# Performance work log

Hardware: AMD Instinct MI355X
Metric: run time of the kernel (lower is better)

Reference implementation:

```python
import jax, jax.numpy as jnp
import numpy as np

N_NODES = 50000
N_EDGES = 800000
IN_FEATS = 128
HEADS = 8
OUT_FEATS = 32
NEG_SLOPE = 0.2


def setup_inputs() -> dict:
    key = jax.random.key(0)
    k_feat, k_w, k_al, k_ar, k_src, k_dst = jax.random.split(key, 6)
    feat = jax.random.normal(k_feat, (N_NODES, IN_FEATS), dtype=jnp.float32)
    W_fc = jax.random.normal(k_w, (HEADS * OUT_FEATS, IN_FEATS), dtype=jnp.float32) * 0.1
    attn_l = jax.random.normal(k_al, (1, HEADS, OUT_FEATS), dtype=jnp.float32) * 0.1
    attn_r = jax.random.normal(k_ar, (1, HEADS, OUT_FEATS), dtype=jnp.float32) * 0.1
    src = jax.random.randint(k_src, (N_EDGES,), 0, N_NODES, dtype=jnp.int32)
    dst = jax.random.randint(k_dst, (N_EDGES,), 0, N_NODES, dtype=jnp.int32)
    return {"feat": feat, "W_fc": W_fc, "attn_l": attn_l, "attn_r": attn_r,
            "src": src, "dst": dst}


def reference(feat, W_fc, attn_l, attn_r, src, dst):
    N = feat.shape[0]
    H, D = attn_l.shape[1], attn_l.shape[2]
    # fc projection: [N, H, D]
    feat_hd = (feat @ W_fc.T).reshape(N, H, D)
    # per-node left/right attention logits: [N, H]
    el = (feat_hd * attn_l).sum(-1)
    er = (feat_hd * attn_r).sum(-1)
    # u_add_v gather -> per-edge score [E, H], then leaky relu
    e = el[src] + er[dst]
    e = jnp.where(e > 0, e, NEG_SLOPE * e)
    # edge softmax: segment softmax over edges grouped by dst node
    m = jax.ops.segment_max(e, dst, num_segments=N)        # [N, H]
    a = jnp.exp(e - m[dst])                                # [E, H]
    z = jax.ops.segment_sum(a, dst, num_segments=N)        # [N, H]
    a = a / z[dst]
    # u_mul_e + sum: weighted scatter-aggregation -> [N, H, D]
    msg = feat_hd[src] * a[:, :, None]                     # [E, H, D]
    out = jax.ops.segment_sum(msg, dst, num_segments=N)
    return out
```

## Files before the change

### kernel.cpp

```cpp
#include <hip/hip_runtime.h>

#define N_NODES_C 50000
#define N_EDGES_C 800000
#define IN_FEATS_C 128
#define HEADS_C 8
#define HD_C 256
#define NEG_SLOPE_C 0.2f
#define SCAN_NBLK 49
#define LDT 136

#define GEMM_BLOCKS 782
#define DEG_BLOCKS 242
#define K1_GRID (GEMM_BLOCKS + DEG_BLOCKS)

typedef __attribute__((ext_vector_type(8))) short bf16x8;
typedef __attribute__((ext_vector_type(4))) float floatx4;

__device__ inline unsigned short f2bf(float f) {
  unsigned int u = __float_as_uint(f);
  unsigned int r = (u + 0x7FFFu + ((u >> 16) & 1u)) >> 16;
  return (unsigned short)r;
}
__device__ inline float bf2f(unsigned short s) {
  unsigned int u = ((unsigned int)s) << 16;
  return __uint_as_float(u);
}

__device__ inline void boff_scan(const int* __restrict__ bsum, int* sboff) {
  int t = threadIdx.x;
  if (t < 64) {
    int own = (t < SCAN_NBLK) ? bsum[t] : 0;
    int v = own;
#pragma unroll
    for (int off = 1; off < 64; off <<= 1) {
      int u = __shfl_up(v, off);
      if (t >= off) v += u;
    }
    sboff[t] = v - own;
  }
  __syncthreads();
}

__global__ __launch_bounds__(256) void prep_kernel(
    const float* __restrict__ W, unsigned short* __restrict__ Wbf,
    int* __restrict__ deg) {
  int b = blockIdx.x, t = threadIdx.x;
  if (b < 32) {
    int i = (b * 256 + t) * 4;
    float4 v = *(const float4*)&W[i];
    ushort4 o;
    o.x = f2bf(v.x); o.y = f2bf(v.y); o.z = f2bf(v.z); o.w = f2bf(v.w);
    *(ushort4*)&Wbf[i] = o;
  } else {
    int i = ((b - 32) * 256 + t) * 4;
    if (i < N_NODES_C) {
      if (i + 4 <= N_NODES_C)
        *(int4*)&deg[i] = make_int4(0, 0, 0, 0);
      else
        for (int k = i; k < N_NODES_C; ++k) deg[k] = 0;
    }
  }
}

__global__ __launch_bounds__(256) void front_kernel(
    const float* __restrict__ feat, const unsigned short* __restrict__ Wbf,
    const float* __restrict__ attn_l, const float* __restrict__ attn_r,
    const int* __restrict__ dst,
    unsigned short* __restrict__ feat_hd_bf,
    float* __restrict__ el, float* __restrict__ er,
    int* __restrict__ deg, int* __restrict__ rank) {
  __shared__ __align__(16) unsigned short sA[128 * LDT];
  __shared__ float sAttnL[128];
  __shared__ float sAttnR[128];
  const int bid = blockIdx.x;
  const int t = threadIdx.x;

  if (bid < DEG_BLOCKS) {
    for (int e0 = (bid * 256 + t) * 8; e0 < N_EDGES_C; e0 += DEG_BLOCKS * 2048) {
      int4 da = *(const int4*)&dst[e0];
      int4 db = *(const int4*)&dst[e0 + 4];
      int r0 = atomicAdd(&deg[da.x], 1);
      int r1 = atomicAdd(&deg[da.y], 1);
      int r2 = atomicAdd(&deg[da.z], 1);
      int r3 = atomicAdd(&deg[da.w], 1);
      int r4 = atomicAdd(&deg[db.x], 1);
      int r5 = atomicAdd(&deg[db.y], 1);
      int r6 = atomicAdd(&deg[db.z], 1);
      int r7 = atomicAdd(&deg[db.w], 1);
      *(int4*)&rank[e0]     = make_int4(r0, r1, r2, r3);
      *(int4*)&rank[e0 + 4] = make_int4(r4, r5, r6, r7);
    }
    return;
  }

  const int gb = bid - DEG_BLOCKS;
  int mt, nt;
  if (gb < 768) {
    mt = ((gb >> 4) << 3) + (gb & 7);
    nt = (gb >> 3) & 1;
  } else {
    int l = gb - 768;
    nt = (l >= 7) ? 1 : 0;
    mt = 384 + (nt ? l - 7 : l);
  }
  const int m0 = mt * 128;
  const int n0 = nt * 128;

  if (t < 128) {
    sAttnL[t] = attn_l[n0 + t];
    sAttnR[t] = attn_r[n0 + t];
  }
#pragma unroll
  for (int i = 0; i < 16; ++i) {
    int idx = t + i * 256;
    int row = idx >> 5;
    int c4 = idx & 31;
    int gn = m0 + row;
    float4 v = (gn < N_NODES_C)
                   ? *(const float4*)&feat[(size_t)gn * IN_FEATS_C + c4 * 4]
                   : make_float4(0.f, 0.f, 0.f, 0.f);
    ushort4 b;
    b.x = f2bf(v.x); b.y = f2bf(v.y); b.z = f2bf(v.z); b.w = f2bf(v.w);
    *(ushort4*)&sA[row * LDT + c4 * 4] = b;
  }
  __syncthreads();

  const int wid = t >> 6;
  const int lane = t & 63;
  const int quad = lane >> 4;
  const int l16 = lane & 15;
  const int wm = (wid & 1) * 64;
  const int wn = (wid >> 1) * 64;

  floatx4 acc[4][4];
#pragma unroll
  for (int i = 0; i < 4; ++i)
#pragma unroll
    for (int j = 0; j < 4; ++j) acc[i][j] = (floatx4){0.f, 0.f, 0.f, 0.f};

#pragma unroll
  for (int ks = 0; ks < 4; ++ks) {
    int k0 = ks * 32 + quad * 8;
    bf16x8 bfv[4];
#pragma unroll
    for (int n2 = 0; n2 < 4; ++n2)
      bfv[n2] = *(const bf16x8*)&Wbf[(size_t)(n0 + wn + n2 * 16 + l16) *
                                         IN_FEATS_C + k0];
    bf16x8 af[4];
#pragma unroll
    for (int m2 = 0; m2 < 4; ++m2)
      af[m2] = *(const bf16x8*)&sA[(wm + m2 * 16 + l16) * LDT + k0];
#pragma unroll
    for (int m2 = 0; m2 < 4; ++m2)
#pragma unroll
      for (int n2 = 0; n2 < 4; ++n2)
        acc[m2][n2] = __builtin_amdgcn_mfma_f32_16x16x32_bf16(
            af[m2], bfv[n2], acc[m2][n2], 0, 0, 0);
  }
  __syncthreads();

#pragma unroll
  for (int m2 = 0; m2 < 4; ++m2)
#pragma unroll
    for (int n2 = 0; n2 < 4; ++n2)
#pragma unroll
      for (int r = 0; r < 4; ++r) {
        int row = wm + m2 * 16 + quad * 4 + r;
        int col = wn + n2 * 16 + l16;
        sA[row * LDT + col] = f2bf(acc[m2][n2][r]);
      }
  __syncthreads();

#pragma unroll
  for (int i = 0; i < 8; ++i) {
    int idx = t + i * 256;
    int row = idx >> 4;
    int ch = idx & 15;
    int gn = m0 + row;
    if (gn < N_NODES_C) {
      *(uint4*)&feat_hd_bf[(size_t)gn * HD_C + n0 + ch * 8] =
          *(const uint4*)&sA[row * LDT + ch * 8];
    }
  }

  {
    int row = t >> 1;
    int hh = t & 1;
    int gn = m0 + row;
    if (gn < N_NODES_C) {
      const unsigned short* pr = &sA[row * LDT + hh * 64];
      const float* al = &sAttnL[hh * 64];
      const float* ar = &sAttnR[hh * 64];
      float el0 = 0.f, el1 = 0.f, er0 = 0.f, er1 = 0.f;
#pragma unroll
      for (int d8 = 0; d8 < 4; ++d8) {
        bf16x8 v0 = *(const bf16x8*)&pr[d8 * 8];
        bf16x8 v1 = *(const bf16x8*)&pr[32 + d8 * 8];
#pragma unroll
        for (int j = 0; j < 8; ++j) {
          float f0 = bf2f((unsigned short)v0[j]);
          float f1 = bf2f((unsigned short)v1[j]);
          el0 = fmaf(f0, al[d8 * 8 + j], el0);
          er0 = fmaf(f0, ar[d8 * 8 + j], er0);
          el1 = fmaf(f1, al[32 + d8 * 8 + j], el1);
          er1 = fmaf(f1, ar[32 + d8 * 8 + j], er1);
        }
      }
      int gh = nt * 4 + hh * 2;
      el[gn * HEADS_C + gh + 0] = el0;
      el[gn * HEADS_C + gh + 1] = el1;
      er[gn * HEADS_C + gh + 0] = er0;
      er[gn * HEADS_C + gh + 1] = er1;
    }
  }
}

__global__ __launch_bounds__(256) void scan1_kernel(
    const int* __restrict__ deg, int2* __restrict__ rsd,
    int* __restrict__ bsum) {
  __shared__ int s[256];
  int b = blockIdx.x, t = threadIdx.x;
  int i0 = b * 1024 + t * 4;
  int d0 = 0, d1 = 0, d2 = 0, d3 = 0;
  if (i0 + 4 <= N_NODES_C) {
    int4 d = *(const int4*)&deg[i0];
    d0 = d.x; d1 = d.y; d2 = d.z; d3 = d.w;
  } else {
    if (i0 + 0 < N_NODES_C) d0 = deg[i0 + 0];
    if (i0 + 1 < N_NODES_C) d1 = deg[i0 + 1];
    if (i0 + 2 < N_NODES_C) d2 = deg[i0 + 2];
    if (i0 + 3 < N_NODES_C) d3 = deg[i0 + 3];
  }
  int l1 = d0, l2 = l1 + d1, l3 = l2 + d2, l4 = l3 + d3;
  s[t] = l4;
  __syncthreads();
#pragma unroll
  for (int off = 1; off < 256; off <<= 1) {
    int add = (t >= off) ? s[t - off] : 0;
    __syncthreads();
    s[t] += add;
    __syncthreads();
  }
  int excl = s[t] - l4;
  if (i0 + 0 < N_NODES_C) rsd[i0 + 0] = make_int2(excl + l1, d0);
  if (i0 + 1 < N_NODES_C) rsd[i0 + 1] = make_int2(excl + l2, d1);
  if (i0 + 2 < N_NODES_C) rsd[i0 + 2] = make_int2(excl + l3, d2);
  if (i0 + 3 < N_NODES_C) rsd[i0 + 3] = make_int2(excl + l4, d3);
  if (t == 255) bsum[b] = s[255];
}

__global__ __launch_bounds__(256) void scatter_kernel(
    const int* __restrict__ src, const int* __restrict__ dst,
    const int2* __restrict__ rsd, const int* __restrict__ bsum,
    const int* __restrict__ rank, int* __restrict__ csr_src) {
  __shared__ int sboff[64];
  boff_scan(bsum, sboff);
  int base = (blockIdx.x * 256 + threadIdx.x) * 4;
  if (base >= N_EDGES_C) return;
  int4 d4 = *(const int4*)&dst[base];
  int4 r4 = *(const int4*)&rank[base];
  int4 s4 = *(const int4*)&src[base];
  int2 v0 = rsd[d4.x];
  int2 v1 = rsd[d4.y];
  int2 v2 = rsd[d4.z];
  int2 v3 = rsd[d4.w];
  csr_src[v0.x - v0.y + sboff[d4.x >> 10] + r4.x] = s4.x;
  csr_src[v1.x - v1.y + sboff[d4.y >> 10] + r4.y] = s4.y;
  csr_src[v2.x - v2.y + sboff[d4.z >> 10] + r4.z] = s4.z;
  csr_src[v3.x - v3.y + sboff[d4.w >> 10] + r4.w] = s4.w;
}

__global__ __launch_bounds__(256) void agg_csr_kernel(
    const unsigned short* __restrict__ feat_hd_bf, const float* __restrict__ el,
    const float* __restrict__ er, const int2* __restrict__ rsd,
    const int* __restrict__ bsum, const int* __restrict__ csr_src,
    float* __restrict__ out) {
  __shared__ int sboff[64];
  boff_scan(bsum, sboff);
  int gid = blockIdx.x * 256 + threadIdx.x;
  int node = gid >> 6;
  int lane = threadIdx.x & 63;
  if (node >= N_NODES_C) return;
  int h = lane >> 3;
  int j8 = lane & 7;
  int hbase = lane & 56;
  int c = lane * 4;
  float er_d = er[node * HEADS_C + h];
  int2 v = rsd[node];
  int dg = v.y;
  int rs = v.x - dg + sboff[node >> 10];
  float4 acc = make_float4(0.f, 0.f, 0.f, 0.f);
  float zsum = 0.f;

  int nb = (dg + 7) >> 3;
  if (nb > 0) {
    const int last = dg - 1;
    int myidx = csr_src[rs + min(j8, last)];
    for (int b = 0; b < nb; ++b) {
      int e0 = b * 8;
      ushort4 f[8];
#pragma unroll
      for (int j = 0; j < 8; ++j) {
        int sj = __shfl(myidx, j);
        f[j] = *(const ushort4*)&feat_hd_bf[(size_t)sj * HD_C + c];
      }
      float x = el[myidx * HEADS_C + h] + er_d;
      x = x > 0.f ? x : NEG_SLOPE_C * x;
      float wv = (e0 + j8 < dg) ? __expf(x) : 0.f;
      int nidx = csr_src[rs + min(e0 + 8 + j8, last)];
      float wj[8];
#pragma unroll
      for (int j = 0; j < 8; ++j) wj[j] = __shfl(wv, hbase + j);
      zsum += ((wj[0] + wj[1]) + (wj[2] + wj[3])) +
              ((wj[4] + wj[5]) + (wj[6] + wj[7]));
#pragma unroll
      for (int j = 0; j < 8; ++j) {
        acc.x = fmaf(wj[j], bf2f(f[j].x), acc.x);
        acc.y = fmaf(wj[j], bf2f(f[j].y), acc.y);
        acc.z = fmaf(wj[j], bf2f(f[j].z), acc.z);
        acc.w = fmaf(wj[j], bf2f(f[j].w), acc.w);
      }
      myidx = nidx;
    }
  }

  float inv = (dg > 0) ? 1.f / zsum : 0.f;
  acc.x *= inv; acc.y *= inv; acc.z *= inv; acc.w *= inv;
  *(float4*)&out[(size_t)node * HD_C + c] = acc;
}

extern "C" void kernel_launch(void* const* d_in, const int* in_sizes, int n_in,
                              void* d_out, int out_size, void* d_ws, size_t ws_size,
                              hipStream_t stream) {
  const float* feat   = (const float*)d_in[0];
  const float* W      = (const float*)d_in[1];
  const float* attn_l = (const float*)d_in[2];
  const float* attn_r = (const float*)d_in[3];
  const int* src      = (const int*)d_in[4];
  const int* dst      = (const int*)d_in[5];
  float* out = (float*)d_out;

  char* ws = (char*)d_ws;
  unsigned short* feat_hd_bf = (unsigned short*)ws;  ws += (size_t)N_NODES_C * HD_C * 2;
  float* el      = (float*)ws;                       ws += (size_t)N_NODES_C * HEADS_C * 4;
  float* er      = (float*)ws;                       ws += (size_t)N_NODES_C * HEADS_C * 4;
  int* deg       = (int*)ws;                         ws += (size_t)N_NODES_C * 4;
  int2* rsd      = (int2*)ws;                        ws += (size_t)N_NODES_C * 8;
  int* bsum      = (int*)ws;                         ws += 64 * 4;
  int* csr_src   = (int*)ws;                         ws += (size_t)N_EDGES_C * 4;
  int* rank      = (int*)ws;                         ws += (size_t)N_EDGES_C * 4;
  unsigned short* Wbf = (unsigned short*)ws;         ws += (size_t)HD_C * IN_FEATS_C * 2;

  prep_kernel<<<81, 256, 0, stream>>>(W, Wbf, deg);

  front_kernel<<<K1_GRID, 256, 0, stream>>>(feat, Wbf, attn_l, attn_r, dst,
                                            feat_hd_bf, el, er, deg, rank);

  scan1_kernel<<<SCAN_NBLK, 256, 0, stream>>>(deg, rsd, bsum);

  scatter_kernel<<<(N_EDGES_C / 4 + 255) / 256, 256, 0, stream>>>(
      src, dst, rsd, bsum, rank, csr_src);

  agg_csr_kernel<<<(N_NODES_C + 3) / 4, 256, 0, stream>>>(
      feat_hd_bf, el, er, rsd, bsum, csr_src, out);
}
```

Before: 222.4 us.

## Co-schedule CSR scatter with projection GEMM in one fused launch

Reorganises the kernel pipeline: the degree histogram and W bf16 conversion now run together in a first kernel (after a memset of deg), the scan runs next, and the CSR scatter blocks are merged with the GEMM/attention-logit blocks into a single mid kernel. The aim is to let the memory/atomic-bound scatter overlap with the compute-bound GEMM, and to take the histogram off the GEMM's critical path. The cost is that the histogram no longer overlaps the GEMM, and the scatter blocks carry the GEMM's large shared-memory footprint, which may limit their occupancy.

After: 226.2 us. No clear change (+1.7%).

```diff
diff --git a/kernel.cpp b/kernel.cpp
--- a/kernel.cpp
+++ b/kernel.cpp
@@ -11,7 +11,10 @@
 
 #define GEMM_BLOCKS 782
 #define DEG_BLOCKS 242
-#define K1_GRID (GEMM_BLOCKS + DEG_BLOCKS)
+#define WCONV_BLOCKS 32
+#define HISTPREP_GRID (DEG_BLOCKS + WCONV_BLOCKS)
+#define SCAT_BLOCKS 782
+#define MID_GRID (SCAT_BLOCKS + GEMM_BLOCKS)
 
 typedef __attribute__((ext_vector_type(8))) short bf16x8;
 typedef __attribute__((ext_vector_type(4))) float floatx4;
@@ -41,59 +44,105 @@
   __syncthreads();
 }
 
-__global__ __launch_bounds__(256) void prep_kernel(
-    const float* __restrict__ W, unsigned short* __restrict__ Wbf,
-    int* __restrict__ deg) {
-  int b = blockIdx.x, t = threadIdx.x;
-  if (b < 32) {
-    int i = (b * 256 + t) * 4;
+__global__ __launch_bounds__(256) void histprep_kernel(
+    const int* __restrict__ dst, const float* __restrict__ W,
+    unsigned short* __restrict__ Wbf, int* __restrict__ deg,
+    int* __restrict__ rank) {
+  const int b = blockIdx.x;
+  const int t = threadIdx.x;
+  if (b >= DEG_BLOCKS) {
+    int i = ((b - DEG_BLOCKS) * 256 + t) * 4;
     float4 v = *(const float4*)&W[i];
     ushort4 o;
     o.x = f2bf(v.x); o.y = f2bf(v.y); o.z = f2bf(v.z); o.w = f2bf(v.w);
     *(ushort4*)&Wbf[i] = o;
+    return;
+  }
+  for (int e0 = (b * 256 + t) * 8; e0 < N_EDGES_C; e0 += DEG_BLOCKS * 2048) {
+    int4 da = *(const int4*)&dst[e0];
+    int4 db = *(const int4*)&dst[e0 + 4];
+    int r0 = atomicAdd(&deg[da.x], 1);
+    int r1 = atomicAdd(&deg[da.y], 1);
+    int r2 = atomicAdd(&deg[da.z], 1);
+    int r3 = atomicAdd(&deg[da.w], 1);
+    int r4 = atomicAdd(&deg[db.x], 1);
+    int r5 = atomicAdd(&deg[db.y], 1);
+    int r6 = atomicAdd(&deg[db.z], 1);
+    int r7 = atomicAdd(&deg[db.w], 1);
+    *(int4*)&rank[e0]     = make_int4(r0, r1, r2, r3);
+    *(int4*)&rank[e0 + 4] = make_int4(r4, r5, r6, r7);
+  }
+}
+
+__global__ __launch_bounds__(256) void scan1_kernel(
+    const int* __restrict__ deg, int2* __restrict__ rsd,
+    int* __restrict__ bsum) {
+  __shared__ int s[256];
+  int b = blockIdx.x, t = threadIdx.x;
+  int i0 = b * 1024 + t * 4;
+  int d0 = 0, d1 = 0, d2 = 0, d3 = 0;
+  if (i0 + 4 <= N_NODES_C) {
+    int4 d = *(const int4*)&deg[i0];
+    d0 = d.x; d1 = d.y; d2 = d.z; d3 = d.w;
   } else {
-    int i = ((b - 32) * 256 + t) * 4;
-    if (i < N_NODES_C) {
-      if (i + 4 <= N_NODES_C)
-        *(int4*)&deg[i] = make_int4(0, 0, 0, 0);
-      else
-        for (int k = i; k < N_NODES_C; ++k) deg[k] = 0;
-    }
-  }
-}
-
-__global__ __launch_bounds__(256) void front_kernel(
+    if (i0 + 0 < N_NODES_C) d0 = deg[i0 + 0];
+    if (i0 + 1 < N_NODES_C) d1 = deg[i0 + 1];
+    if (i0 + 2 < N_NODES_C) d2 = deg[i0 + 2];
+    if (i0 + 3 < N_NODES_C) d3 = deg[i0 + 3];
+  }
+  int l1 = d0, l2 = l1 + d1, l3 = l2 + d2, l4 = l3 + d3;
+  s[t] = l4;
+  __syncthreads();
+#pragma unroll
+  for (int off = 1; off < 256; off <<= 1) {
+    int add = (t >= off) ? s[t - off] : 0;
+    __syncthreads();
+    s[t] += add;
+    __syncthreads();
+  }
+  int excl = s[t] - l4;
+  if (i0 + 0 < N_NODES_C) rsd[i0 + 0] = make_int2(excl + l1, d0);
+  if (i0 + 1 < N_NODES_C) rsd[i0 + 1] = make_int2(excl + l2, d1);
+  if (i0 + 2 < N_NODES_C) rsd[i0 + 2] = make_int2(excl + l3, d2);
+  if (i0 + 3 < N_NODES_C) rsd[i0 + 3] = make_int2(excl + l4, d3);
+  if (t == 255) bsum[b] = s[255];
+}
+
+__global__ __launch_bounds__(256) void mid_kernel(
     const float* __restrict__ feat, const unsigned short* __restrict__ Wbf,
     const float* __restrict__ attn_l, const float* __restrict__ attn_r,
-    const int* __restrict__ dst,
+    const int* __restrict__ src, const int* __restrict__ dst,
+    const int2* __restrict__ rsd, const int* __restrict__ bsum,
+    const int* __restrict__ rank,
     unsigned short* __restrict__ feat_hd_bf,
     float* __restrict__ el, float* __restrict__ er,
-    int* __restrict__ deg, int* __restrict__ rank) {
+    int* __restrict__ csr_src) {
   __shared__ __align__(16) unsigned short sA[128 * LDT];
   __shared__ float sAttnL[128];
   __shared__ float sAttnR[128];
+  __shared__ int sboff[64];
   const int bid = blockIdx.x;
   const int t = threadIdx.x;
 
-  if (bid < DEG_BLOCKS) {
-    for (int e0 = (bid * 256 + t) * 8; e0 < N_EDGES_C; e0 += DEG_BLOCKS * 2048) {
-      int4 da = *(const int4*)&dst[e0];
-      int4 db = *(const int4*)&dst[e0 + 4];
-      int r0 = atomicAdd(&deg[da.x], 1);
-      int r1 = atomicAdd(&deg[da.y], 1);
-      int r2 = atomicAdd(&deg[da.z], 1);
-      int r3 = atomicAdd(&deg[da.w], 1);
-      int r4 = atomicAdd(&deg[db.x], 1);
-      int r5 = atomicAdd(&deg[db.y], 1);
-      int r6 = atomicAdd(&deg[db.z], 1);
-      int r7 = atomicAdd(&deg[db.w], 1);
-      *(int4*)&rank[e0]     = make_int4(r0, r1, r2, r3);
-      *(int4*)&rank[e0 + 4] = make_int4(r4, r5, r6, r7);
-    }
+  if (bid < SCAT_BLOCKS) {
+    boff_scan(bsum, sboff);
+    int base = (bid * 256 + t) * 4;
+    if (base >= N_EDGES_C) return;
+    int4 d4 = *(const int4*)&dst[base];
+    int4 r4 = *(const int4*)&rank[base];
+    int4 s4 = *(const int4*)&src[base];
+    int2 v0 = rsd[d4.x];
+    int2 v1 = rsd[d4.y];
+    int2 v2 = rsd[d4.z];
+    int2 v3 = rsd[d4.w];
+    csr_src[v0.x - v0.y + sboff[d4.x >> 10] + r4.x] = s4.x;
+    csr_src[v1.x - v1.y + sboff[d4.y >> 10] + r4.y] = s4.y;
+    csr_src[v2.x - v2.y + sboff[d4.z >> 10] + r4.z] = s4.z;
+    csr_src[v3.x - v3.y + sboff[d4.w >> 10] + r4.w] = s4.w;
     return;
   }
 
-  const int gb = bid - DEG_BLOCKS;
+  const int gb = bid - SCAT_BLOCKS;
   int mt, nt;
   if (gb < 768) {
     mt = ((gb >> 4) << 3) + (gb & 7);
@@ -213,61 +262,6 @@
       er[gn * HEADS_C + gh + 1] = er1;
     }
   }
-}
-
-__global__ __launch_bounds__(256) void scan1_kernel(
-    const int* __restrict__ deg, int2* __restrict__ rsd,
-    int* __restrict__ bsum) {
-  __shared__ int s[256];
-  int b = blockIdx.x, t = threadIdx.x;
-  int i0 = b * 1024 + t * 4;
-  int d0 = 0, d1 = 0, d2 = 0, d3 = 0;
-  if (i0 + 4 <= N_NODES_C) {
-    int4 d = *(const int4*)&deg[i0];
-    d0 = d.x; d1 = d.y; d2 = d.z; d3 = d.w;
-  } else {
-    if (i0 + 0 < N_NODES_C) d0 = deg[i0 + 0];
-    if (i0 + 1 < N_NODES_C) d1 = deg[i0 + 1];
-    if (i0 + 2 < N_NODES_C) d2 = deg[i0 + 2];
-    if (i0 + 3 < N_NODES_C) d3 = deg[i0 + 3];
-  }
-  int l1 = d0, l2 = l1 + d1, l3 = l2 + d2, l4 = l3 + d3;
-  s[t] = l4;
-  __syncthreads();
-#pragma unroll
-  for (int off = 1; off < 256; off <<= 1) {
-    int add = (t >= off) ? s[t - off] : 0;
-    __syncthreads();
-    s[t] += add;
-    __syncthreads();
-  }
-  int excl = s[t] - l4;
-  if (i0 + 0 < N_NODES_C) rsd[i0 + 0] = make_int2(excl + l1, d0);
-  if (i0 + 1 < N_NODES_C) rsd[i0 + 1] = make_int2(excl + l2, d1);
-  if (i0 + 2 < N_NODES_C) rsd[i0 + 2] = make_int2(excl + l3, d2);
-  if (i0 + 3 < N_NODES_C) rsd[i0 + 3] = make_int2(excl + l4, d3);
-  if (t == 255) bsum[b] = s[255];
-}
-
-__global__ __launch_bounds__(256) void scatter_kernel(
-    const int* __restrict__ src, const int* __restrict__ dst,
-    const int2* __restrict__ rsd, const int* __restrict__ bsum,
-    const int* __restrict__ rank, int* __restrict__ csr_src) {
-  __shared__ int sboff[64];
-  boff_scan(bsum, sboff);
-  int base = (blockIdx.x * 256 + threadIdx.x) * 4;
-  if (base >= N_EDGES_C) return;
-  int4 d4 = *(const int4*)&dst[base];
-  int4 r4 = *(const int4*)&rank[base];
-  int4 s4 = *(const int4*)&src[base];
-  int2 v0 = rsd[d4.x];
-  int2 v1 = rsd[d4.y];
-  int2 v2 = rsd[d4.z];
-  int2 v3 = rsd[d4.w];
-  csr_src[v0.x - v0.y + sboff[d4.x >> 10] + r4.x] = s4.x;
-  csr_src[v1.x - v1.y + sboff[d4.y >> 10] + r4.y] = s4.y;
-  csr_src[v2.x - v2.y + sboff[d4.z >> 10] + r4.z] = s4.z;
-  csr_src[v3.x - v3.y + sboff[d4.w >> 10] + r4.w] = s4.w;
 }
 
 __global__ __launch_bounds__(256) void agg_csr_kernel(
@@ -351,15 +345,15 @@
   int* rank      = (int*)ws;                         ws += (size_t)N_EDGES_C * 4;
   unsigned short* Wbf = (unsigned short*)ws;         ws += (size_t)HD_C * IN_FEATS_C * 2;
 
-  prep_kernel<<<81, 256, 0, stream>>>(W, Wbf, deg);
-
-  front_kernel<<<K1_GRID, 256, 0, stream>>>(feat, Wbf, attn_l, attn_r, dst,
-                                            feat_hd_bf, el, er, deg, rank);
+  hipMemsetAsync(deg, 0, (size_t)N_NODES_C * 4, stream);
+
+  histprep_kernel<<<HISTPREP_GRID, 256, 0, stream>>>(dst, W, Wbf, deg, rank);
 
   scan1_kernel<<<SCAN_NBLK, 256, 0, stream>>>(deg, rsd, bsum);
 
-  scatter_kernel<<<(N_EDGES_C / 4 + 255) / 256, 256, 0, stream>>>(
-      src, dst, rsd, bsum, rank, csr_src);
+  mid_kernel<<<MID_GRID, 256, 0, stream>>>(feat, Wbf, attn_l, attn_r, src, dst,
+                                           rsd, bsum, rank, feat_hd_bf, el, er,
+                                           csr_src);
 
   agg_csr_kernel<<<(N_NODES_C + 3) / 4, 256, 0, stream>>>(
       feat_hd_bf, el, er, rsd, bsum, csr_src, out);
```

## Compute full 256-column output per GEMM block with 512 threads

Applied to the files above, without the earlier changes.

Each GEMM block now covers all 256 output columns for a 128-row tile using 8 wavefronts, instead of two blocks each computing 128 columns. The feature tile is loaded from global memory and converted to bf16 once rather than twice, and the epilogue writes results through shared memory in two halves with extra barriers. The degree-histogram blocks are resized to 512 threads with a single pass each. This halves feature reloads and block count, but larger blocks lower occupancy flexibility and add synchronisation in the epilogue.

Measured after the change: 227.8 us. 2.4% more time.

```diff
diff --git a/kernel.cpp b/kernel.cpp
--- a/kernel.cpp
+++ b/kernel.cpp
@@ -9,9 +9,9 @@
 #define SCAN_NBLK 49
 #define LDT 136
 
-#define GEMM_BLOCKS 782
-#define DEG_BLOCKS 242
-#define K1_GRID (GEMM_BLOCKS + DEG_BLOCKS)
+#define GEMM2_BLOCKS 391
+#define HIST2_BLOCKS 196
+#define FRONT2_GRID (HIST2_BLOCKS + GEMM2_BLOCKS)
 
 typedef __attribute__((ext_vector_type(8))) short bf16x8;
 typedef __attribute__((ext_vector_type(4))) float floatx4;
@@ -62,7 +62,7 @@
   }
 }
 
-__global__ __launch_bounds__(256) void front_kernel(
+__global__ __launch_bounds__(512) void front2_kernel(
     const float* __restrict__ feat, const unsigned short* __restrict__ Wbf,
     const float* __restrict__ attn_l, const float* __restrict__ attn_r,
     const int* __restrict__ dst,
@@ -70,13 +70,14 @@
     float* __restrict__ el, float* __restrict__ er,
     int* __restrict__ deg, int* __restrict__ rank) {
   __shared__ __align__(16) unsigned short sA[128 * LDT];
-  __shared__ float sAttnL[128];
-  __shared__ float sAttnR[128];
+  __shared__ float sAttnL[256];
+  __shared__ float sAttnR[256];
   const int bid = blockIdx.x;
   const int t = threadIdx.x;
 
-  if (bid < DEG_BLOCKS) {
-    for (int e0 = (bid * 256 + t) * 8; e0 < N_EDGES_C; e0 += DEG_BLOCKS * 2048) {
+  if (bid < HIST2_BLOCKS) {
+    int e0 = (bid * 512 + t) * 8;
+    if (e0 < N_EDGES_C) {
       int4 da = *(const int4*)&dst[e0];
       int4 db = *(const int4*)&dst[e0 + 4];
       int r0 = atomicAdd(&deg[da.x], 1);
@@ -93,26 +94,15 @@
     return;
   }
 
-  const int gb = bid - DEG_BLOCKS;
-  int mt, nt;
-  if (gb < 768) {
-    mt = ((gb >> 4) << 3) + (gb & 7);
-    nt = (gb >> 3) & 1;
-  } else {
-    int l = gb - 768;
-    nt = (l >= 7) ? 1 : 0;
-    mt = 384 + (nt ? l - 7 : l);
-  }
-  const int m0 = mt * 128;
-  const int n0 = nt * 128;
-
-  if (t < 128) {
-    sAttnL[t] = attn_l[n0 + t];
-    sAttnR[t] = attn_r[n0 + t];
-  }
-#pragma unroll
-  for (int i = 0; i < 16; ++i) {
-    int idx = t + i * 256;
+  const int m0 = (bid - HIST2_BLOCKS) * 128;
+
+  if (t < 256) {
+    sAttnL[t] = attn_l[t];
+    sAttnR[t] = attn_r[t];
+  }
+#pragma unroll
+  for (int i = 0; i < 8; ++i) {
+    int idx = t + i * 512;
     int row = idx >> 5;
     int c4 = idx & 31;
     int gn = m0 + row;
@@ -144,7 +134,7 @@
     bf16x8 bfv[4];
 #pragma unroll
     for (int n2 = 0; n2 < 4; ++n2)
-      bfv[n2] = *(const bf16x8*)&Wbf[(size_t)(n0 + wn + n2 * 16 + l16) *
+      bfv[n2] = *(const bf16x8*)&Wbf[(size_t)(wn + n2 * 16 + l16) *
                                          IN_FEATS_C + k0];
     bf16x8 af[4];
 #pragma unroll
@@ -160,58 +150,65 @@
   __syncthreads();
 
 #pragma unroll
-  for (int m2 = 0; m2 < 4; ++m2)
-#pragma unroll
-    for (int n2 = 0; n2 < 4; ++n2)
-#pragma unroll
-      for (int r = 0; r < 4; ++r) {
-        int row = wm + m2 * 16 + quad * 4 + r;
-        int col = wn + n2 * 16 + l16;
-        sA[row * LDT + col] = f2bf(acc[m2][n2][r]);
+  for (int half = 0; half < 2; ++half) {
+    if ((wn >> 7) == half) {
+      int wcol = wn & 127;
+#pragma unroll
+      for (int m2 = 0; m2 < 4; ++m2)
+#pragma unroll
+        for (int n2 = 0; n2 < 4; ++n2)
+#pragma unroll
+          for (int r = 0; r < 4; ++r) {
+            int row = wm + m2 * 16 + quad * 4 + r;
+            int col = wcol + n2 * 16 + l16;
+            sA[row * LDT + col] = f2bf(acc[m2][n2][r]);
+          }
+    }
+    __syncthreads();
+
+#pragma unroll
+    for (int i = 0; i < 4; ++i) {
+      int idx = t + i * 512;
+      int row = idx >> 4;
+      int ch = idx & 15;
+      int gn = m0 + row;
+      if (gn < N_NODES_C) {
+        *(uint4*)&feat_hd_bf[(size_t)gn * HD_C + half * 128 + ch * 8] =
+            *(const uint4*)&sA[row * LDT + ch * 8];
       }
-  __syncthreads();
-
-#pragma unroll
-  for (int i = 0; i < 8; ++i) {
-    int idx = t + i * 256;
-    int row = idx >> 4;
-    int ch = idx & 15;
-    int gn = m0 + row;
-    if (gn < N_NODES_C) {
-      *(uint4*)&feat_hd_bf[(size_t)gn * HD_C + n0 + ch * 8] =
-          *(const uint4*)&sA[row * LDT + ch * 8];
-    }
-  }
-
-  {
-    int row = t >> 1;
-    int hh = t & 1;
-    int gn = m0 + row;
-    if (gn < N_NODES_C) {
-      const unsigned short* pr = &sA[row * LDT + hh * 64];
-      const float* al = &sAttnL[hh * 64];
-      const float* ar = &sAttnR[hh * 64];
-      float el0 = 0.f, el1 = 0.f, er0 = 0.f, er1 = 0.f;
-#pragma unroll
-      for (int d8 = 0; d8 < 4; ++d8) {
-        bf16x8 v0 = *(const bf16x8*)&pr[d8 * 8];
-        bf16x8 v1 = *(const bf16x8*)&pr[32 + d8 * 8];
-#pragma unroll
-        for (int j = 0; j < 8; ++j) {
-          float f0 = bf2f((unsigned short)v0[j]);
-          float f1 = bf2f((unsigned short)v1[j]);
-          el0 = fmaf(f0, al[d8 * 8 + j], el0);
-          er0 = fmaf(f0, ar[d8 * 8 + j], er0);
-          el1 = fmaf(f1, al[32 + d8 * 8 + j], el1);
-          er1 = fmaf(f1, ar[32 + d8 * 8 + j], er1);
+    }
+
+    if (t < 256) {
+      int row = t >> 1;
+      int hh = t & 1;
+      int gn = m0 + row;
+      if (gn < N_NODES_C) {
+        const unsigned short* pr = &sA[row * LDT + hh * 64];
+        const float* al = &sAttnL[half * 128 + hh * 64];
+        const float* ar = &sAttnR[half * 128 + hh * 64];
+        float el0 = 0.f, el1 = 0.f, er0 = 0.f, er1 = 0.f;
+#pragma unroll
+        for (int d8 = 0; d8 < 4; ++d8) {
+          bf16x8 v0 = *(const bf16x8*)&pr[d8 * 8];
+          bf16x8 v1 = *(const bf16x8*)&pr[32 + d8 * 8];
+#pragma unroll
+          for (int j = 0; j < 8; ++j) {
+            float f0 = bf2f((unsigned short)v0[j]);
+            float f1 = bf2f((unsigned short)v1[j]);
+            el0 = fmaf(f0, al[d8 * 8 + j], el0);
+            er0 = fmaf(f0, ar[d8 * 8 + j], er0);
+            el1 = fmaf(f1, al[32 + d8 * 8 + j], el1);
+            er1 = fmaf(f1, ar[32 + d8 * 8 + j], er1);
+          }
         }
+        int gh = half * 4 + hh * 2;
+        el[gn * HEADS_C + gh + 0] = el0;
+        el[gn * HEADS_C + gh + 1] = el1;
+        er[gn * HEADS_C + gh + 0] = er0;
+        er[gn * HEADS_C + gh + 1] = er1;
       }
-      int gh = nt * 4 + hh * 2;
-      el[gn * HEADS_C + gh + 0] = el0;
-      el[gn * HEADS_C + gh + 1] = el1;
-      er[gn * HEADS_C + gh + 0] = er0;
-      er[gn * HEADS_C + gh + 1] = er1;
-    }
+    }
+    __syncthreads();
   }
 }
 
@@ -353,8 +350,8 @@
 
   prep_kernel<<<81, 256, 0, stream>>>(W, Wbf, deg);
 
-  front_kernel<<<K1_GRID, 256, 0, stream>>>(feat, Wbf, attn_l, attn_r, dst,
-                                            feat_hd_bf, el, er, deg, rank);
+  front2_kernel<<<FRONT2_GRID, 512, 0, stream>>>(feat, Wbf, attn_l, attn_r, dst,
+                                                 feat_hd_bf, el, er, deg, rank);
 
   scan1_kernel<<<SCAN_NBLK, 256, 0, stream>>>(deg, rsd, bsum);
 
```

## Store features head-major and aggregate one wavefront per node-head pair

Applied to the files above, without the earlier changes.

The projection kernel now writes bf16 features and el/er logits in a head-major transposed layout. The aggregation kernel assigns each wavefront a single (node, head) pair, with 8 lanes per edge slot covering the 32 head channels, and reduces across edge slots with xor shuffles. The per-head feature table is smaller and may stay cache-resident during random gathers, and csr_src reads use nontemporal loads. In exchange, the grid is 8× larger and the per-node setup (CSR offsets, block-offset scan, index loads) is repeated for every head.

New measurement: 349.3 us. 57.0% more time.

```diff
diff --git a/kernel.cpp b/kernel.cpp
--- a/kernel.cpp
+++ b/kernel.cpp
@@ -66,8 +66,8 @@
     const float* __restrict__ feat, const unsigned short* __restrict__ Wbf,
     const float* __restrict__ attn_l, const float* __restrict__ attn_r,
     const int* __restrict__ dst,
-    unsigned short* __restrict__ feat_hd_bf,
-    float* __restrict__ el, float* __restrict__ er,
+    unsigned short* __restrict__ feat_hd_T,
+    float* __restrict__ el_T, float* __restrict__ er_T,
     int* __restrict__ deg, int* __restrict__ rank) {
   __shared__ __align__(16) unsigned short sA[128 * LDT];
   __shared__ float sAttnL[128];
@@ -178,7 +178,10 @@
     int ch = idx & 15;
     int gn = m0 + row;
     if (gn < N_NODES_C) {
-      *(uint4*)&feat_hd_bf[(size_t)gn * HD_C + n0 + ch * 8] =
+      int gc = n0 + ch * 8;
+      int hh2 = gc >> 5;
+      int co = gc & 31;
+      *(uint4*)&feat_hd_T[((size_t)hh2 * N_NODES_C + gn) * 32 + co] =
           *(const uint4*)&sA[row * LDT + ch * 8];
     }
   }
@@ -207,10 +210,10 @@
         }
       }
       int gh = nt * 4 + hh * 2;
-      el[gn * HEADS_C + gh + 0] = el0;
-      el[gn * HEADS_C + gh + 1] = el1;
-      er[gn * HEADS_C + gh + 0] = er0;
-      er[gn * HEADS_C + gh + 1] = er1;
+      el_T[(size_t)(gh + 0) * N_NODES_C + gn] = el0;
+      el_T[(size_t)(gh + 1) * N_NODES_C + gn] = el1;
+      er_T[(size_t)(gh + 0) * N_NODES_C + gn] = er0;
+      er_T[(size_t)(gh + 1) * N_NODES_C + gn] = er1;
     }
   }
 }
@@ -271,21 +274,22 @@
 }
 
 __global__ __launch_bounds__(256) void agg_csr_kernel(
-    const unsigned short* __restrict__ feat_hd_bf, const float* __restrict__ el,
-    const float* __restrict__ er, const int2* __restrict__ rsd,
+    const unsigned short* __restrict__ feat_hd_T, const float* __restrict__ el_T,
+    const float* __restrict__ er_T, const int2* __restrict__ rsd,
     const int* __restrict__ bsum, const int* __restrict__ csr_src,
     float* __restrict__ out) {
   __shared__ int sboff[64];
   boff_scan(bsum, sboff);
-  int gid = blockIdx.x * 256 + threadIdx.x;
-  int node = gid >> 6;
-  int lane = threadIdx.x & 63;
+  const int bid = blockIdx.x;
+  const int h = bid & 7;
+  const int node = (bid >> 3) * 4 + (threadIdx.x >> 6);
   if (node >= N_NODES_C) return;
-  int h = lane >> 3;
-  int j8 = lane & 7;
-  int hbase = lane & 56;
-  int c = lane * 4;
-  float er_d = er[node * HEADS_C + h];
+  const int lane = threadIdx.x & 63;
+  const int j8 = lane >> 3;
+  const int c8 = lane & 7;
+  const unsigned short* fh = feat_hd_T + (size_t)h * N_NODES_C * 32;
+  const float* elh = el_T + (size_t)h * N_NODES_C;
+  float er_d = er_T[(size_t)h * N_NODES_C + node];
   int2 v = rsd[node];
   int dg = v.y;
   int rs = v.x - dg + sboff[node >> 10];
@@ -295,38 +299,37 @@
   int nb = (dg + 7) >> 3;
   if (nb > 0) {
     const int last = dg - 1;
-    int myidx = csr_src[rs + min(j8, last)];
+    int myidx = __builtin_nontemporal_load(&csr_src[rs + min(j8, last)]);
     for (int b = 0; b < nb; ++b) {
       int e0 = b * 8;
-      ushort4 f[8];
-#pragma unroll
-      for (int j = 0; j < 8; ++j) {
-        int sj = __shfl(myidx, j);
-        f[j] = *(const ushort4*)&feat_hd_bf[(size_t)sj * HD_C + c];
-      }
-      float x = el[myidx * HEADS_C + h] + er_d;
+      ushort4 f = *(const ushort4*)&fh[(size_t)myidx * 32 + c8 * 4];
+      float x = elh[myidx] + er_d;
       x = x > 0.f ? x : NEG_SLOPE_C * x;
-      float wv = (e0 + j8 < dg) ? __expf(x) : 0.f;
-      int nidx = csr_src[rs + min(e0 + 8 + j8, last)];
-      float wj[8];
-#pragma unroll
-      for (int j = 0; j < 8; ++j) wj[j] = __shfl(wv, hbase + j);
-      zsum += ((wj[0] + wj[1]) + (wj[2] + wj[3])) +
-              ((wj[4] + wj[5]) + (wj[6] + wj[7]));
-#pragma unroll
-      for (int j = 0; j < 8; ++j) {
-        acc.x = fmaf(wj[j], bf2f(f[j].x), acc.x);
-        acc.y = fmaf(wj[j], bf2f(f[j].y), acc.y);
-        acc.z = fmaf(wj[j], bf2f(f[j].z), acc.z);
-        acc.w = fmaf(wj[j], bf2f(f[j].w), acc.w);
-      }
+      float w = (e0 + j8 < dg) ? __expf(x) : 0.f;
+      int nidx = __builtin_nontemporal_load(
+          &csr_src[rs + min(e0 + 8 + j8, last)]);
+      zsum += w;
+      acc.x = fmaf(w, bf2f(f.x), acc.x);
+      acc.y = fmaf(w, bf2f(f.y), acc.y);
+      acc.z = fmaf(w, bf2f(f.z), acc.z);
+      acc.w = fmaf(w, bf2f(f.w), acc.w);
       myidx = nidx;
     }
+#pragma unroll
+    for (int off = 8; off < 64; off <<= 1) {
+      zsum += __shfl_xor(zsum, off);
+      acc.x += __shfl_xor(acc.x, off);
+      acc.y += __shfl_xor(acc.y, off);
+      acc.z += __shfl_xor(acc.z, off);
+      acc.w += __shfl_xor(acc.w, off);
+    }
   }
 
   float inv = (dg > 0) ? 1.f / zsum : 0.f;
-  acc.x *= inv; acc.y *= inv; acc.z *= inv; acc.w *= inv;
-  *(float4*)&out[(size_t)node * HD_C + c] = acc;
+  if (j8 == 0) {
+    *(float4*)&out[(size_t)node * HD_C + h * 32 + c8 * 4] =
+        make_float4(acc.x * inv, acc.y * inv, acc.z * inv, acc.w * inv);
+  }
 }
 
 extern "C" void kernel_launch(void* const* d_in, const int* in_sizes, int n_in,
@@ -341,9 +344,9 @@
   float* out = (float*)d_out;
 
   char* ws = (char*)d_ws;
-  unsigned short* feat_hd_bf = (unsigned short*)ws;  ws += (size_t)N_NODES_C * HD_C * 2;
-  float* el      = (float*)ws;                       ws += (size_t)N_NODES_C * HEADS_C * 4;
-  float* er      = (float*)ws;                       ws += (size_t)N_NODES_C * HEADS_C * 4;
+  unsigned short* feat_hd_T = (unsigned short*)ws;   ws += (size_t)N_NODES_C * HD_C * 2;
+  float* el_T    = (float*)ws;                       ws += (size_t)N_NODES_C * HEADS_C * 4;
+  float* er_T    = (float*)ws;                       ws += (size_t)N_NODES_C * HEADS_C * 4;
   int* deg       = (int*)ws;                         ws += (size_t)N_NODES_C * 4;
   int2* rsd      = (int2*)ws;                        ws += (size_t)N_NODES_C * 8;
   int* bsum      = (int*)ws;                         ws += 64 * 4;
@@ -354,13 +357,13 @@
   prep_kernel<<<81, 256, 0, stream>>>(W, Wbf, deg);
 
   front_kernel<<<K1_GRID, 256, 0, stream>>>(feat, Wbf, attn_l, attn_r, dst,
-                                            feat_hd_bf, el, er, deg, rank);
+                                            feat_hd_T, el_T, er_T, deg, rank);
 
   scan1_kernel<<<SCAN_NBLK, 256, 0, stream>>>(deg, rsd, bsum);
 
   scatter_kernel<<<(N_EDGES_C / 4 + 255) / 256, 256, 0, stream>>>(
       src, dst, rsd, bsum, rank, csr_src);
 
-  agg_csr_kernel<<<(N_NODES_C + 3) / 4, 256, 0, stream>>>(
-      feat_hd_bf, el, er, rsd, bsum, csr_src, out);
-}
+  agg_csr_kernel<<<8 * ((N_NODES_C + 3) / 4), 256, 0, stream>>>(
+      feat_hd_T, el_T, er_T, rsd, bsum, csr_src, out);
+}
```
